# Optimization experiments

Hardware: AMD Instinct MI355X
Metric: run time of the kernel (lower is better)

## Reference

```python
import jax, jax.numpy as jnp
import numpy as np

N, M, E, HID, H = 50000, 4000, 320000, 128, 2
EPS = 1e-5  # torch BatchNorm1d eps


def _lrelu(x):
    return jnp.where(x >= 0, x, 0.2 * x)


def _bn(x, g, b):
    # BatchNorm1d in training mode: biased batch statistics over dim 0
    m = x.mean(0)
    v = ((x - m) ** 2).mean(0)
    return g * (x - m) * jax.lax.rsqrt(v + EPS) + b


def _seg_softmax(a, idx, n):
    # softmax of a[E,heads] normalized per node index idx (PyG softmax)
    mx = jax.ops.segment_max(a, idx, num_segments=n)
    e = jnp.exp(a - mx[idx])
    s = jax.ops.segment_sum(e, idx, num_segments=n)
    return e / s[idx]


def _hgconv(x, he_n, he_e, he_w, W, att, bias, heads):
    # PyG HypergraphConv(use_attention=True, concat=False)
    xl = (x @ W).reshape(N, heads, HID)                  # lin(x) -> [N,heads,C]
    # hyperedge_attr = incidence^T @ x  (matches to_dense_adj path in HGAT)
    ea = jax.ops.segment_sum(x[he_n], he_e, num_segments=M)  # [M,F]
    eal = (ea @ W).reshape(M, heads, HID)                # lin(hyperedge_attr)
    a = (jnp.concatenate([xl[he_n], eal[he_e]], axis=-1) * att[0]).sum(-1)  # [E,heads]
    a = _seg_softmax(_lrelu(a), he_n, N)
    # degree normalizations
    Dn = jax.ops.segment_sum(he_w[he_e], he_n, num_segments=N)
    Dinv = jnp.where(Dn > 0, 1.0 / Dn, 0.0)
    Bn = jax.ops.segment_sum(jnp.ones((E,), x.dtype), he_e, num_segments=M)
    Binv = jnp.where(Bn > 0, 1.0 / Bn, 0.0)
    # node -> hyperedge
    m1 = Binv[he_e][:, None, None] * xl[he_n] * a[..., None]
    eo = jax.ops.segment_sum(m1, he_e, num_segments=M)   # [M,heads,C]
    # hyperedge -> node
    m2 = Dinv[he_n][:, None, None] * eo[he_e] * a[..., None]
    out = jax.ops.segment_sum(m2, he_n, num_segments=N)  # [N,heads,C]
    return out.mean(1) + bias                            # concat=False -> head mean


def _forward(x, he_w, lin1_w, lin1_b, bn1_g, bn1_b, h1_w, h1_att, h1_b,
             bn2_g, bn2_b, h2_w, h2_att, h2_b, bn3_g, bn3_b,
             lin2_w, lin2_b, bn4_g, bn4_b, he_n, he_e):
    src = x
    x = _bn(_lrelu(x @ lin1_w + lin1_b), bn1_g, bn1_b)
    x2 = _hgconv(x, he_n, he_e, he_w, h1_w, h1_att, h1_b, H)
    x = _bn(x + x2, bn2_g, bn2_b)
    x2 = _hgconv(x, he_n, he_e, he_w, h2_w, h2_att, h2_b, 1)
    x = _bn(x + x2, bn3_g, bn3_b)
    x = _lrelu(x @ lin2_w + lin2_b)
    return _bn(src + x, bn4_g, bn4_b)


def setup_inputs() -> dict:
    key = jax.random.key(0)
    ks = jax.random.split(key, 10)
    s = 0.05
    he_n = jax.random.randint(ks[0], (E,), 0, N, dtype=jnp.int32)
    he_e = (jnp.arange(E, dtype=jnp.int32) % M)  # every hyperedge id used
    return {
        'x': jax.random.normal(ks[1], (N, 128), jnp.float32),
        'he_n': he_n, 'he_e': he_e,
        'he_w': jnp.ones((M,), jnp.float32),
        'lin1_w': jax.random.normal(ks[2], (128, HID), jnp.float32) * s,
        'lin1_b': jnp.zeros((HID,), jnp.float32),
        'bn1_g': jnp.ones((HID,), jnp.float32), 'bn1_b': jnp.zeros((HID,), jnp.float32),
        'h1_w': jax.random.normal(ks[3], (HID, H * HID), jnp.float32) * s,
        'h1_att': jax.random.normal(ks[4], (1, H, 2 * HID), jnp.float32) * s,
        'h1_b': jnp.zeros((HID,), jnp.float32),
        'bn2_g': jnp.ones((HID,), jnp.float32), 'bn2_b': jnp.zeros((HID,), jnp.float32),
        'h2_w': jax.random.normal(ks[5], (HID, HID), jnp.float32) * s,
        'h2_att': jax.random.normal(ks[6], (1, 1, 2 * HID), jnp.float32) * s,
        'h2_b': jnp.zeros((HID,), jnp.float32),
        'bn3_g': jnp.ones((HID,), jnp.float32), 'bn3_b': jnp.zeros((HID,), jnp.float32),
        'lin2_w': jax.random.normal(ks[7], (HID, 128), jnp.float32) * s,
        'lin2_b': jnp.zeros((128,), jnp.float32),
        'bn4_g': jnp.ones((128,), jnp.float32), 'bn4_b': jnp.zeros((128,), jnp.float32),
    }


def reference(x, he_n, he_e, he_w, lin1_w, lin1_b, bn1_g, bn1_b, h1_w, h1_att, h1_b,
              bn2_g, bn2_b, h2_w, h2_att, h2_b, bn3_g, bn3_b,
              lin2_w, lin2_b, bn4_g, bn4_b):
    return _forward(x, he_w, lin1_w, lin1_b, bn1_g, bn1_b, h1_w, h1_att, h1_b,
                    bn2_g, bn2_b, h2_w, h2_att, h2_b, bn3_g, bn3_b,
                    lin2_w, lin2_b, bn4_g, bn4_b, he_n, he_e)
```

## Files before the change

### kernel.cpp

```cpp
#include <hip/hip_runtime.h>
#include <math.h>

constexpr int Nn = 50000;
constexpr int Mm = 4000;
constexpr int Ee = 320000;
constexpr int KPB = Ee / Mm;
constexpr float BINV = 1.0f / (float)KPB;
constexpr float EPSf = 1e-5f;
constexpr int NBKT = 16;
constexpr int NBSCAN = 49;

__device__ __forceinline__ float lrelu_f(float x) { return x >= 0.f ? x : 0.2f * x; }

__device__ __forceinline__ float wave_sum(float v) {
#pragma unroll
    for (int o = 32; o >= 1; o >>= 1) v += __shfl_xor(v, o, 64);
    return v;
}

__device__ __forceinline__ void finalize_to_lds(const float* __restrict__ st,
                                                const float* __restrict__ g,
                                                const float* __restrict__ b,
                                                float* ABsh, int t) {
    if (t < 128) {
        double ds = 0, dq = 0;
#pragma unroll
        for (int i = 0; i < NBKT; i++) {
            ds += (double)st[i * 256 + t];
            dq += (double)st[i * 256 + 128 + t];
        }
        double mean = ds / (double)Nn;
        double var = dq / (double)Nn - mean * mean;
        float rstd = (float)(1.0 / sqrt(var + (double)EPSf));
        float A = g[t] * rstd;
        ABsh[t] = A;
        ABsh[128 + t] = b[t] - (float)mean * A;
    }
    __syncthreads();
}

__device__ void scan_body(const int* __restrict__ counts, int* __restrict__ offs,
                          int b, int t) {
    __shared__ int sdi[256];
    int pre = 0;
    for (int i = t; i < b * 1024; i += 256) pre += counts[i];
    sdi[t] = pre;
    __syncthreads();
    for (int st = 128; st >= 1; st >>= 1) {
        if (t < st) sdi[t] += sdi[t + st];
        __syncthreads();
    }
    int run0 = sdi[0];
    __syncthreads();
    int c4[4];
    int s = 0;
#pragma unroll
    for (int i = 0; i < 4; i++) {
        int n = b * 1024 + t * 4 + i;
        c4[i] = (n < Nn) ? counts[n] : 0;
        s += c4[i];
    }
    sdi[t] = s;
    __syncthreads();
    for (int off = 1; off < 256; off <<= 1) {
        int v = (t >= off) ? sdi[t - off] : 0;
        __syncthreads();
        sdi[t] += v;
        __syncthreads();
    }
    int run = sdi[t] - s + run0;
#pragma unroll
    for (int i = 0; i < 4; i++) {
        int n = b * 1024 + t * 4 + i;
        if (n < Nn) offs[n] = run;
        run += c4[i];
    }
    if (b == NBSCAN - 1 && t == 255) offs[Nn] = run0 + sdi[255];
}

template <int ROWS, bool LRELU, bool PROBN, bool RESID, bool STATS, bool PACKH2, bool SCANX>
__global__ __launch_bounds__(256) void gemmT(const float* __restrict__ A, size_t aystride,
                                             const float* __restrict__ B, int ldb,
                                             const float* __restrict__ bias, float scale,
                                             const float* __restrict__ stIn,
                                             const float* __restrict__ fing,
                                             const float* __restrict__ finb,
                                             const float* __restrict__ resid,
                                             float* __restrict__ stF,
                                             float* __restrict__ C, int ldc, int R,
                                             int gemmBlocksX,
                                             const int* __restrict__ counts,
                                             int* __restrict__ offs) {
    constexpr int RPT = ROWS / 16;
    const int t = threadIdx.x;
    if (SCANX && (int)blockIdx.x >= gemmBlocksX) {
        if (blockIdx.y == 0) scan_body(counts, offs, blockIdx.x - gemmBlocksX, t);
        return;
    }
    __shared__ float As[16][ROWS + 4];
    __shared__ float Bs[16][128];
    __shared__ float Sred[STATS ? 16 : 1][STATS ? 128 : 1];
    __shared__ float ABsh[PROBN ? 256 : 1];
    const int ty = t >> 4, tx = t & 15;
    const int row0 = blockIdx.x * ROWS;
    const int bcol = blockIdx.y * 128;
    A += (size_t)blockIdx.y * aystride;

    if (PROBN) finalize_to_lds(stIn, fing, finb, ABsh, t);

    float4 acc[RPT][2];
#pragma unroll
    for (int i = 0; i < RPT; i++)
#pragma unroll
        for (int q = 0; q < 2; q++) acc[i][q] = make_float4(0.f, 0.f, 0.f, 0.f);

    for (int k0 = 0; k0 < 128; k0 += 16) {
        if (ROWS == 64) {
            int r = t >> 2, kc = (t & 3) * 4;
            int rr = row0 + r;
            rr = rr < R ? rr : R - 1;
            float4 av = *(const float4*)(A + (size_t)rr * 128 + k0 + kc);
            if (PROBN) {
                float4 sA = *(const float4*)&ABsh[k0 + kc];
                float4 sB = *(const float4*)&ABsh[128 + k0 + kc];
                av.x = av.x * sA.x + sB.x; av.y = av.y * sA.y + sB.y;
                av.z = av.z * sA.z + sB.z; av.w = av.w * sA.w + sB.w;
            }
            As[kc + 0][r] = av.x; As[kc + 1][r] = av.y;
            As[kc + 2][r] = av.z; As[kc + 3][r] = av.w;
        } else {
            int r = t >> 3, kc = (t & 7) * 2;
            int rr = row0 + r;
            rr = rr < R ? rr : R - 1;
            float2 av = *(const float2*)(A + (size_t)rr * 128 + k0 + kc);
            if (PROBN) {
                av.x = av.x * ABsh[k0 + kc] + ABsh[128 + k0 + kc];
                av.y = av.y * ABsh[k0 + kc + 1] + ABsh[128 + k0 + kc + 1];
            }
            As[kc + 0][r] = av.x;
            As[kc + 1][r] = av.y;
        }
        {
            int kk = t >> 5, c4 = (t & 31) * 4;
            float4 bv0 = *(const float4*)(B + (size_t)(k0 + kk) * ldb + bcol + c4);
            float4 bv1 = *(const float4*)(B + (size_t)(k0 + kk + 8) * ldb + bcol + c4);
            *(float4*)&Bs[kk][c4] = bv0;
            *(float4*)&Bs[kk + 8][c4] = bv1;
        }
        __syncthreads();
#pragma unroll
        for (int kk = 0; kk < 16; kk++) {
            float ar[RPT];
            if (RPT == 4) {
                float4 a4 = *(const float4*)&As[kk][ty * 4];
                ar[0] = a4.x; ar[1] = a4.y; ar[2] = a4.z; ar[3] = a4.w;
            } else {
                float2 a2 = *(const float2*)&As[kk][ty * 2];
                ar[0] = a2.x; ar[RPT - 1] = a2.y;
            }
            float4 b0 = *(const float4*)&Bs[kk][4 * tx];
            float4 b1 = *(const float4*)&Bs[kk][64 + 4 * tx];
#pragma unroll
            for (int i = 0; i < RPT; i++) {
                acc[i][0].x = fmaf(ar[i], b0.x, acc[i][0].x);
                acc[i][0].y = fmaf(ar[i], b0.y, acc[i][0].y);
                acc[i][0].z = fmaf(ar[i], b0.z, acc[i][0].z);
                acc[i][0].w = fmaf(ar[i], b0.w, acc[i][0].w);
                acc[i][1].x = fmaf(ar[i], b1.x, acc[i][1].x);
                acc[i][1].y = fmaf(ar[i], b1.y, acc[i][1].y);
                acc[i][1].z = fmaf(ar[i], b1.z, acc[i][1].z);
                acc[i][1].w = fmaf(ar[i], b1.w, acc[i][1].w);
            }
        }
        __syncthreads();
    }

    float4 bv0 = make_float4(0.f, 0.f, 0.f, 0.f), bv1 = bv0;
    if (bias) {
        bv0 = *(const float4*)(bias + bcol + 4 * tx);
        bv1 = *(const float4*)(bias + bcol + 64 + 4 * tx);
    }
    float4 cs0 = make_float4(0.f, 0.f, 0.f, 0.f), cs1 = cs0, cq0 = cs0, cq1 = cs0;
#pragma unroll
    for (int i = 0; i < RPT; i++) {
        int row = row0 + ty * RPT + i;
        if (row >= R) continue;
        float4 v0, v1;
        v0.x = acc[i][0].x * scale + bv0.x; v0.y = acc[i][0].y * scale + bv0.y;
        v0.z = acc[i][0].z * scale + bv0.z; v0.w = acc[i][0].w * scale + bv0.w;
        v1.x = acc[i][1].x * scale + bv1.x; v1.y = acc[i][1].y * scale + bv1.y;
        v1.z = acc[i][1].z * scale + bv1.z; v1.w = acc[i][1].w * scale + bv1.w;
        if (LRELU) {
            v0.x = lrelu_f(v0.x); v0.y = lrelu_f(v0.y); v0.z = lrelu_f(v0.z); v0.w = lrelu_f(v0.w);
            v1.x = lrelu_f(v1.x); v1.y = lrelu_f(v1.y); v1.z = lrelu_f(v1.z); v1.w = lrelu_f(v1.w);
        }
        if (RESID) {
            float4 r0 = *(const float4*)(resid + (size_t)row * 128 + bcol + 4 * tx);
            float4 r1 = *(const float4*)(resid + (size_t)row * 128 + bcol + 64 + 4 * tx);
            v0.x += r0.x; v0.y += r0.y; v0.z += r0.z; v0.w += r0.w;
            v1.x += r1.x; v1.y += r1.y; v1.z += r1.z; v1.w += r1.w;
        }
        if (PACKH2) {
            int h = blockIdx.y;
            float* c0 = C + (size_t)row * ldc + 8 * tx + 2 * h;
            *(float2*)(c0) = make_float2(v0.x, v0.y);
            *(float2*)(c0 + 4) = make_float2(v0.z, v0.w);
            float* c1 = C + (size_t)row * ldc + 128 + 8 * tx + 2 * h;
            *(float2*)(c1) = make_float2(v1.x, v1.y);
            *(float2*)(c1 + 4) = make_float2(v1.z, v1.w);
        } else {
            *(float4*)(C + (size_t)row * ldc + bcol + 4 * tx) = v0;
            *(float4*)(C + (size_t)row * ldc + bcol + 64 + 4 * tx) = v1;
        }
        if (STATS) {
            cs0.x += v0.x; cs0.y += v0.y; cs0.z += v0.z; cs0.w += v0.w;
            cs1.x += v1.x; cs1.y += v1.y; cs1.z += v1.z; cs1.w += v1.w;
            cq0.x += v0.x * v0.x; cq0.y += v0.y * v0.y; cq0.z += v0.z * v0.z; cq0.w += v0.w * v0.w;
            cq1.x += v1.x * v1.x; cq1.y += v1.y * v1.y; cq1.z += v1.z * v1.z; cq1.w += v1.w * v1.w;
        }
    }
    if (STATS) {
        int bkt = blockIdx.x & (NBKT - 1);
#pragma unroll
        for (int pass = 0; pass < 2; pass++) {
            *(float4*)&Sred[ty][4 * tx] = pass ? cq0 : cs0;
            *(float4*)&Sred[ty][64 + 4 * tx] = pass ? cq1 : cs1;
            __syncthreads();
            if (t < 128) {
                float tot = 0.f;
#pragma unroll
                for (int r = 0; r < 16; r++) tot += Sred[r][t];
                atomicAdd(&stF[bkt * 256 + pass * 128 + t], tot);
            }
            __syncthreads();
        }
    }
}

__global__ void count_edges_watt(const int* __restrict__ he_n, int* __restrict__ counts,
                                 const float* __restrict__ h1_w, const float* __restrict__ h1_att,
                                 const float* __restrict__ h2_w, const float* __restrict__ h2_att,
                                 float* __restrict__ wnA, float* __restrict__ weA) {
    int t = threadIdx.x;
    if (blockIdx.x == 1250) {
        for (int j = 0; j < 3; j++) {
            int id = t + 256 * j;
            if (id >= 768) break;
            int which = id / 384;
            int rem = id % 384;
            int h3 = rem >> 7, k = rem & 127;
            float s = 0.f;
            if (h3 < 2) {
                const float* wrow = h1_w + (size_t)k * 256 + h3 * 128;
                const float* arow = h1_att + h3 * 256 + which * 128;
                for (int c = 0; c < 128; c++) s += wrow[c] * arow[c];
            } else {
                const float* wrow = h2_w + (size_t)k * 128;
                const float* arow = h2_att + which * 128;
                for (int c = 0; c < 128; c++) s += wrow[c] * arow[c];
            }
            (which ? weA : wnA)[h3 * 128 + k] = s;
        }
        return;
    }
    int e = blockIdx.x * 256 + t;
    if (e < Ee) atomicAdd(&counts[he_n[e]], 1);
}

template <int H, bool FILL>
__global__ __launch_bounds__(256) void bn_dots(const float* __restrict__ X,
                                               const float* __restrict__ stIn,
                                               const float* __restrict__ fing,
                                               const float* __restrict__ finb,
                                               float* __restrict__ ABout,
                                               const float* __restrict__ wn,
                                               const float* __restrict__ we,
                                               float* __restrict__ an,
                                               float* __restrict__ pe,
                                               const int* __restrict__ he_n,
                                               const int* __restrict__ offs,
                                               int* __restrict__ cursor,
                                               int* __restrict__ eid, int mainBlocks) {
    int t = threadIdx.x;
    if (FILL && (int)blockIdx.x >= mainBlocks) {
        int e = (blockIdx.x - mainBlocks) * 256 + t;
        if (e < Ee) {
            int n = he_n[e];
            int p = atomicAdd(&cursor[n], 1);
            eid[offs[n] + p] = e;
        }
        return;
    }
    __shared__ float ABsh[256];
    finalize_to_lds(stIn, fing, finb, ABsh, t);
    if (blockIdx.x == 0) ABout[t] = ABsh[t];
    int w = t >> 6, lane = t & 63;
    float a0 = ABsh[lane], a1 = ABsh[lane + 64];
    float b0 = ABsh[128 + lane], b1 = ABsh[192 + lane];
    float wn0[H], wn1[H], we0[H], we1[H];
#pragma unroll
    for (int h = 0; h < H; h++) {
        wn0[h] = wn[h * 128 + lane]; wn1[h] = wn[h * 128 + 64 + lane];
        we0[h] = we[h * 128 + lane]; we1[h] = we[h * 128 + 64 + lane];
    }
#pragma unroll
    for (int nn = 0; nn < 4; nn++) {
        int row = blockIdx.x * 16 + w * 4 + nn;
        const float* xr = X + (size_t)row * 128;
        float v0 = xr[lane] * a0 + b0;
        float v1 = xr[lane + 64] * a1 + b1;
        float pv[H], qv[H];
#pragma unroll
        for (int h = 0; h < H; h++) {
            pv[h] = wave_sum(v0 * wn0[h] + v1 * wn1[h]);
            qv[h] = wave_sum(v0 * we0[h] + v1 * we1[h]);
        }
        if (lane == 0) {
            if (H == 2) {
                *(float2*)&an[row * 2] = make_float2(pv[0], pv[1]);
                *(float2*)&pe[row * 2] = make_float2(qv[0], qv[1]);
            } else {
                an[row] = pv[0];
                pe[row] = qv[0];
            }
        }
    }
}

__global__ __launch_bounds__(256) void bn_out(const float* __restrict__ X,
                                              const float* __restrict__ stIn,
                                              const float* __restrict__ fing,
                                              const float* __restrict__ finb,
                                              float* __restrict__ Y) {
    __shared__ float ABsh[256];
    int t = threadIdx.x;
    finalize_to_lds(stIn, fing, finb, ABsh, t);
    int w = t >> 6, lane = t & 63;
    float a0 = ABsh[lane], a1 = ABsh[lane + 64];
    float b0 = ABsh[128 + lane], b1 = ABsh[192 + lane];
#pragma unroll
    for (int nn = 0; nn < 4; nn++) {
        int row = blockIdx.x * 16 + w * 4 + nn;
        const float* xr = X + (size_t)row * 128;
        float* yr = Y + (size_t)row * 128;
        yr[lane] = xr[lane] * a0 + b0;
        yr[lane + 64] = xr[lane + 64] * a1 + b1;
    }
}

template <int H>
__global__ __launch_bounds__(256) void ea_from_pe(const int* __restrict__ he_n,
                                                  const float* __restrict__ pe,
                                                  float* __restrict__ ae) {
    int w = threadIdx.x >> 6, lane = threadIdx.x & 63;
    int m = blockIdx.x * 4 + w;
    if (m >= Mm) return;
    float s[H];
#pragma unroll
    for (int h = 0; h < H; h++) s[h] = 0.f;
    for (int k = lane; k < KPB; k += 64) {
        int idx = he_n[m + k * Mm];
        if (H == 2) {
            float2 p2 = *(const float2*)(pe + (size_t)idx * 2);
            s[0] += p2.x;
            s[H - 1] += p2.y;
        } else {
            s[0] += pe[idx];
        }
    }
#pragma unroll
    for (int h = 0; h < H; h++) s[h] = wave_sum(s[h]);
    if (lane == 0)
#pragma unroll
        for (int h = 0; h < H; h++) ae[m * H + h] = s[h];
}

template <int H>
__global__ __launch_bounds__(256) void seg_softmax(const int* __restrict__ offs,
                                                   const int* __restrict__ eid,
                                                   const float* __restrict__ an,
                                                   const float* __restrict__ ae,
                                                   const float* __restrict__ he_w,
                                                   float* __restrict__ aw,
                                                   float* __restrict__ sdl) {
    int t = threadIdx.x;
    int wv = t >> 6, lane = t & 63;
    int q = lane >> 3, li = lane & 7;
    int n = blockIdx.x * 32 + wv * 8 + q;
    bool valid = n < Nn;
    int base = valid ? offs[n] : 0;
    int deg = valid ? offs[n + 1] - base : 0;
    float anv[H];
#pragma unroll
    for (int h = 0; h < H; h++) anv[h] = valid ? an[n * H + h] : 0.f;

    bool h0 = li < deg, h1 = li + 8 < deg;
    int e0 = 0, e1 = 0, m0 = 0, m1 = 0;
    float l0[H], l1[H];
    float mx[H];
#pragma unroll
    for (int h = 0; h < H; h++) { mx[h] = -INFINITY; l0[h] = 0.f; l1[h] = 0.f; }
    if (h0) {
        e0 = eid[base + li];
        m0 = e0 % Mm;
#pragma unroll
        for (int h = 0; h < H; h++) {
            l0[h] = lrelu_f(anv[h] + ae[m0 * H + h]);
            mx[h] = fmaxf(mx[h], l0[h]);
        }
    }
    if (h1) {
        e1 = eid[base + li + 8];
        m1 = e1 % Mm;
#pragma unroll
        for (int h = 0; h < H; h++) {
            l1[h] = lrelu_f(anv[h] + ae[m1 * H + h]);
            mx[h] = fmaxf(mx[h], l1[h]);
        }
    }
    for (int c = li + 16; c < deg; c += 8) {
        int e = eid[base + c];
        int m = e % Mm;
#pragma unroll
        for (int h = 0; h < H; h++) mx[h] = fmaxf(mx[h], lrelu_f(anv[h] + ae[m * H + h]));
    }
#pragma unroll
    for (int h = 0; h < H; h++) {
#pragma unroll
        for (int o = 1; o <= 4; o <<= 1) mx[h] = fmaxf(mx[h], __shfl_xor(mx[h], o, 64));
    }
    float sm[H], p0[H], p1[H];
#pragma unroll
    for (int h = 0; h < H; h++) { sm[h] = 0.f; p0[h] = 0.f; p1[h] = 0.f; }
    float dn = 0.f;
    if (h0) {
        dn += he_w[m0];
#pragma unroll
        for (int h = 0; h < H; h++) { p0[h] = expf(l0[h] - mx[h]); sm[h] += p0[h]; }
    }
    if (h1) {
        dn += he_w[m1];
#pragma unroll
        for (int h = 0; h < H; h++) { p1[h] = expf(l1[h] - mx[h]); sm[h] += p1[h]; }
    }
    for (int c = li + 16; c < deg; c += 8) {
        int e = eid[base + c];
        int m = e % Mm;
        dn += he_w[m];
#pragma unroll
        for (int h = 0; h < H; h++) sm[h] += expf(lrelu_f(anv[h] + ae[m * H + h]) - mx[h]);
    }
#pragma unroll
    for (int o = 1; o <= 4; o <<= 1) dn += __shfl_xor(dn, o, 64);
#pragma unroll
    for (int h = 0; h < H; h++) {
#pragma unroll
        for (int o = 1; o <= 4; o <<= 1) sm[h] += __shfl_xor(sm[h], o, 64);
    }
    float Dv = dn > 0.f ? 1.0f / dn : 0.0f;
    float premul = Dv * (H == 2 ? 0.5f : 1.0f);
    if (h0) {
        float p[H];
#pragma unroll
        for (int h = 0; h < H; h++) p[h] = p0[h] / sm[h];
        if (H == 2) {
            *(float2*)(aw + (size_t)e0 * 2) = make_float2(p[0], p[1]);
            *(float4*)(sdl + (size_t)(base + li) * 4) =
                make_float4(__int_as_float(m0), p[0] * premul, p[H - 1] * premul, 0.f);
        } else {
            aw[e0] = p[0];
            *(float2*)(sdl + (size_t)(base + li) * 2) = make_float2(__int_as_float(m0), p[0] * premul);
        }
    }
    if (h1) {
        float p[H];
#pragma unroll
        for (int h = 0; h < H; h++) p[h] = p1[h] / sm[h];
        if (H == 2) {
            *(float2*)(aw + (size_t)e1 * 2) = make_float2(p[0], p[1]);
            *(float4*)(sdl + (size_t)(base + li + 8) * 4) =
                make_float4(__int_as_float(m1), p[0] * premul, p[H - 1] * premul, 0.f);
        } else {
            aw[e1] = p[0];
            *(float2*)(sdl + (size_t)(base + li + 8) * 2) =
                make_float2(__int_as_float(m1), p[0] * premul);
        }
    }
    for (int c = li + 16; c < deg; c += 8) {
        int e = eid[base + c];
        int m = e % Mm;
        float p[H];
#pragma unroll
        for (int h = 0; h < H; h++) p[h] = expf(lrelu_f(anv[h] + ae[m * H + h]) - mx[h]) / sm[h];
        if (H == 2) {
            *(float2*)(aw + (size_t)e * 2) = make_float2(p[0], p[1]);
            *(float4*)(sdl + (size_t)(base + c) * 4) =
                make_float4(__int_as_float(m), p[0] * premul, p[H - 1] * premul, 0.f);
        } else {
            aw[e] = p[0];
            *(float2*)(sdl + (size_t)(base + c) * 2) = make_float2(__int_as_float(m), p[0] * premul);
        }
    }
}

template <int H>
__global__ __launch_bounds__(256) void s_build(const float* __restrict__ X,
                                               const float* __restrict__ AB,
                                               const int* __restrict__ he_n,
                                               const float* __restrict__ aw,
                                               float* __restrict__ S) {
    __shared__ int idx[KPB];
    __shared__ float av[KPB][H];
    __shared__ float red[8][H][128];
    int m = blockIdx.x, t = threadIdx.x;
    int g = t >> 5, l = t & 31;
    if (t < KPB) idx[t] = he_n[m + t * Mm];
    for (int q2 = t; q2 < KPB * H; q2 += 256) {
        int k = q2 / H, h = q2 - k * H;
        av[k][h] = aw[(size_t)(m + k * Mm) * H + h];
    }
    __syncthreads();
    float4 A4 = ((const float4*)AB)[l];
    float4 B4 = ((const float4*)(AB + 128))[l];
    float4 acc[H];
#pragma unroll
    for (int h = 0; h < H; h++) acc[h] = make_float4(0.f, 0.f, 0.f, 0.f);
#pragma unroll
    for (int kk = 0; kk < KPB / 8; kk++) {
        int k = g + kk * 8;
        float4 v = ((const float4*)(X + (size_t)idx[k] * 128))[l];
        v.x = v.x * A4.x + B4.x;
        v.y = v.y * A4.y + B4.y;
        v.z = v.z * A4.z + B4.z;
        v.w = v.w * A4.w + B4.w;
#pragma unroll
        for (int h = 0; h < H; h++) {
            float a = av[k][h];
            acc[h].x = fmaf(a, v.x, acc[h].x);
            acc[h].y = fmaf(a, v.y, acc[h].y);
            acc[h].z = fmaf(a, v.z, acc[h].z);
            acc[h].w = fmaf(a, v.w, acc[h].w);
        }
    }
#pragma unroll
    for (int h = 0; h < H; h++) *(float4*)&red[g][h][l * 4] = acc[h];
    __syncthreads();
    if (t < 32 * H) {
        int h = t >> 5, l2 = t & 31;
        float4 s = make_float4(0.f, 0.f, 0.f, 0.f);
#pragma unroll
        for (int gg = 0; gg < 8; gg++) {
            float4 r = *(const float4*)&red[gg][h][l2 * 4];
            s.x += r.x; s.y += r.y; s.z += r.z; s.w += r.w;
        }
        ((float4*)(S + ((size_t)h * Mm + m) * 128))[l2] = s;
    }
}

template <int H>
__global__ __launch_bounds__(256) void node_agg(const int* __restrict__ offs,
                                                const float* __restrict__ sdl,
                                                const float* __restrict__ eo,
                                                const float* __restrict__ bias,
                                                const float* __restrict__ AB,
                                                float* __restrict__ stF,
                                                float* __restrict__ T) {
    __shared__ float smem[4][256];
    __shared__ float redS[4][128], redQ[4][128];
    int t = threadIdx.x;
    int w = t >> 6, lane = t & 63;
    int n0 = blockIdx.x * 16 + w * 4;
    int o = offs[n0 + (lane < 4 ? lane : 4)];
    int b0 = __shfl(o, 0, 64);
    int b1 = __shfl(o, 1, 64);
    int b2 = __shfl(o, 2, 64);
    int b3 = __shfl(o, 3, 64);
    int b4 = __shfl(o, 4, 64);
    int cnt = b4 - b0;
    int cnt64 = cnt < 64 ? cnt : 64;

    if (lane < cnt64) {
        int slot = b0 + lane;
        if (H == 2) {
            *(float4*)&smem[w][4 * lane] = *(const float4*)(sdl + (size_t)slot * 4);
        } else {
            *(float2*)&smem[w][2 * lane] = *(const float2*)(sdl + (size_t)slot * 2);
        }
    }
    __syncthreads();

    int s1 = min(b1 - b0, cnt64), s2 = min(b2 - b0, cnt64), s3 = min(b3 - b0, cnt64);
    float2 acc0 = make_float2(0.f, 0.f), acc1 = acc0, acc2 = acc0, acc3 = acc0;

#define NA_BODY(ACC, CBEG, CEND)                                                \
    {                                                                           \
        int c = (CBEG);                                                         \
        for (; c + 1 < (CEND); c += 2) {                                        \
            if (H == 2) {                                                       \
                float4 sa = *(const float4*)&smem[w][4 * c];                    \
                float4 sb = *(const float4*)&smem[w][4 * (c + 1)];              \
                float4 ea = *(const float4*)(eo + (size_t)__float_as_int(sa.x) * 256 + 4 * lane); \
                float4 eb = *(const float4*)(eo + (size_t)__float_as_int(sb.x) * 256 + 4 * lane); \
                ACC.x += sa.y * ea.x + sa.z * ea.z + sb.y * eb.x + sb.z * eb.z; \
                ACC.y += sa.y * ea.y + sa.z * ea.w + sb.y * eb.y + sb.z * eb.w; \
            } else {                                                            \
                float2 sa = *(const float2*)&smem[w][2 * c];                    \
                float2 sb = *(const float2*)&smem[w][2 * (c + 1)];              \
                float2 ea = *(const float2*)(eo + (size_t)__float_as_int(sa.x) * 128 + 2 * lane); \
                float2 eb = *(const float2*)(eo + (size_t)__float_as_int(sb.x) * 128 + 2 * lane); \
                ACC.x += sa.y * ea.x + sb.y * eb.x;                             \
                ACC.y += sa.y * ea.y + sb.y * eb.y;                             \
            }                                                                   \
        }                                                                       \
        if (c < (CEND)) {                                                       \
            if (H == 2) {                                                       \
                float4 sa = *(const float4*)&smem[w][4 * c];                    \
                float4 ea = *(const float4*)(eo + (size_t)__float_as_int(sa.x) * 256 + 4 * lane); \
                ACC.x += sa.y * ea.x + sa.z * ea.z;                             \
                ACC.y += sa.y * ea.y + sa.z * ea.w;                             \
            } else {                                                            \
                float2 sa = *(const float2*)&smem[w][2 * c];                    \
                float2 ea = *(const float2*)(eo + (size_t)__float_as_int(sa.x) * 128 + 2 * lane); \
                ACC.x += sa.y * ea.x;                                           \
                ACC.y += sa.y * ea.y;                                           \
            }                                                                   \
        }                                                                       \
    }
    NA_BODY(acc0, 0, s1)
    NA_BODY(acc1, s1, s2)
    NA_BODY(acc2, s2, s3)
    NA_BODY(acc3, s3, cnt64)
#undef NA_BODY

    for (int ss = 64; ss < cnt; ss++) {
        int slot = b0 + ss;
        int j = (slot >= b1) + (slot >= b2) + (slot >= b3);
        float cx, cy;
        if (H == 2) {
            float4 v = *(const float4*)(sdl + (size_t)slot * 4);
            float4 ev = *(const float4*)(eo + (size_t)__float_as_int(v.x) * 256 + 4 * lane);
            cx = v.y * ev.x + v.z * ev.z;
            cy = v.y * ev.y + v.z * ev.w;
        } else {
            float2 v = *(const float2*)(sdl + (size_t)slot * 2);
            float2 ev = *(const float2*)(eo + (size_t)__float_as_int(v.x) * 128 + 2 * lane);
            cx = v.y * ev.x;
            cy = v.y * ev.y;
        }
        if (j == 0) { acc0.x += cx; acc0.y += cy; }
        else if (j == 1) { acc1.x += cx; acc1.y += cy; }
        else if (j == 2) { acc2.x += cx; acc2.y += cy; }
        else { acc3.x += cx; acc3.y += cy; }
    }

    int col = 2 * lane;
    float2 A2 = *(const float2*)(AB + col);
    float2 B2 = *(const float2*)(AB + 128 + col);
    float2 bi = *(const float2*)(bias + col);
    float cs0 = 0.f, cs1 = 0.f, cq0 = 0.f, cq1 = 0.f;
    float2 accs[4] = {acc0, acc1, acc2, acc3};
#pragma unroll
    for (int j = 0; j < 4; j++) {
        int n = n0 + j;
        float2 xr = *(const float2*)(T + (size_t)n * 128 + col);
        float r0 = xr.x * A2.x + B2.x + bi.x + accs[j].x;
        float r1 = xr.y * A2.y + B2.y + bi.y + accs[j].y;
        *(float2*)(T + (size_t)n * 128 + col) = make_float2(r0, r1);
        cs0 += r0; cs1 += r1;
        cq0 += r0 * r0; cq1 += r1 * r1;
    }
    redS[w][col] = cs0; redS[w][col + 1] = cs1;
    redQ[w][col] = cq0; redQ[w][col + 1] = cq1;
    __syncthreads();
    if (t < 128) {
        float s = 0.f, qq = 0.f;
#pragma unroll
        for (int ww = 0; ww < 4; ww++) { s += redS[ww][t]; qq += redQ[ww][t]; }
        int bkt = blockIdx.x & (NBKT - 1);
        atomicAdd(&stF[bkt * 256 + t], s);
        atomicAdd(&stF[bkt * 256 + 128 + t], qq);
    }
}

extern "C" void kernel_launch(void* const* d_in, const int* in_sizes, int n_in,
                              void* d_out, int out_size, void* d_ws, size_t ws_size,
                              hipStream_t stream) {
    const float* x = (const float*)d_in[0];
    const int* he_n = (const int*)d_in[1];
    const float* he_w = (const float*)d_in[3];
    const float* lin1_w = (const float*)d_in[4];
    const float* lin1_b = (const float*)d_in[5];
    const float* bn1_g = (const float*)d_in[6];
    const float* bn1_b = (const float*)d_in[7];
    const float* h1_w = (const float*)d_in[8];
    const float* h1_att = (const float*)d_in[9];
    const float* h1_b = (const float*)d_in[10];
    const float* bn2_g = (const float*)d_in[11];
    const float* bn2_b = (const float*)d_in[12];
    const float* h2_w = (const float*)d_in[13];
    const float* h2_att = (const float*)d_in[14];
    const float* h2_b = (const float*)d_in[15];
    const float* bn3_g = (const float*)d_in[16];
    const float* bn3_b = (const float*)d_in[17];
    const float* lin2_w = (const float*)d_in[18];
    const float* lin2_b = (const float*)d_in[19];
    const float* bn4_g = (const float*)d_in[20];
    const float* bn4_b = (const float*)d_in[21];
    float* out = (float*)d_out;

    char* ws = (char*)d_ws;
    size_t off = 0;
    auto alloc = [&](size_t bytes) -> char* {
        char* p = ws + off;
        off = (off + bytes + 255) & ~(size_t)255;
        return p;
    };
    int* counts = (int*)alloc((size_t)Nn * 4);
    int* cursor = (int*)alloc((size_t)Nn * 4);
    float* stats = (float*)alloc((size_t)4 * NBKT * 256 * 4);
    size_t zbytes = off;
    int* offs = (int*)alloc((size_t)(Nn + 1) * 4);
    int* eid = (int*)alloc((size_t)Ee * 4);
    float* an = (float*)alloc((size_t)Nn * 2 * 4);
    float* pe = (float*)alloc((size_t)Nn * 2 * 4);
    float* ae = (float*)alloc((size_t)Mm * 2 * 4);
    float* aw = (float*)alloc((size_t)Ee * 2 * 4);
    float* sdl = (float*)alloc((size_t)Ee * 4 * 4);
    float* S = (float*)alloc((size_t)2 * Mm * 128 * 4);
    float* eo = (float*)alloc((size_t)2 * Mm * 128 * 4);
    float* wnA = (float*)alloc(384 * 4);
    float* weA = (float*)alloc(384 * 4);
    float* AB = (float*)alloc(2 * 256 * 4);
    float* buf = (float*)alloc((size_t)Nn * 128 * 4);

    float* st0 = stats;
    float* st1 = stats + NBKT * 256;
    float* st2 = stats + 2 * NBKT * 256;
    float* st3 = stats + 3 * NBKT * 256;
    float *AB1 = AB, *AB2 = AB + 256;

    hipMemsetAsync(d_ws, 0, zbytes, stream);

    constexpr int GB32 = (Nn + 31) / 32;
    count_edges_watt<<<1251, 256, 0, stream>>>(he_n, counts, h1_w, h1_att, h2_w, h2_att,
                                               wnA, weA);

    gemmT<32, true, false, false, true, false, true><<<dim3(GB32 + NBSCAN, 1), 256, 0, stream>>>(
        x, 0, lin1_w, 128, lin1_b, 1.f, nullptr, nullptr, nullptr, nullptr, st0, buf, 128, Nn,
        GB32, counts, offs);
    bn_dots<2, true><<<3125 + 1250, 256, 0, stream>>>(buf, st0, bn1_g, bn1_b, AB1, wnA, weA,
                                                      an, pe, he_n, offs, cursor, eid, 3125);

    ea_from_pe<2><<<Mm / 4, 256, 0, stream>>>(he_n, pe, ae);
    seg_softmax<2><<<(Nn + 31) / 32, 256, 0, stream>>>(offs, eid, an, ae, he_w, aw, sdl);
    s_build<2><<<Mm, 256, 0, stream>>>(buf, AB1, he_n, aw, S);
    gemmT<32, false, false, false, false, true, false><<<dim3(125, 2), 256, 0, stream>>>(
        S, (size_t)Mm * 128, h1_w, 256, nullptr, BINV, nullptr, nullptr, nullptr, nullptr,
        nullptr, eo, 256, Mm, 125, nullptr, nullptr);
    node_agg<2><<<3125, 256, 0, stream>>>(offs, sdl, eo, h1_b, AB1, st1, buf);

    bn_dots<1, false><<<3125, 256, 0, stream>>>(buf, st1, bn2_g, bn2_b, AB2, wnA + 256,
                                                weA + 256, an, pe, nullptr, nullptr, nullptr,
                                                nullptr, 3125);

    ea_from_pe<1><<<Mm / 4, 256, 0, stream>>>(he_n, pe, ae);
    seg_softmax<1><<<(Nn + 31) / 32, 256, 0, stream>>>(offs, eid, an, ae, he_w, aw, sdl);
    s_build<1><<<Mm, 256, 0, stream>>>(buf, AB2, he_n, aw, S);
    gemmT<32, false, false, false, false, false, false><<<dim3(125, 1), 256, 0, stream>>>(
        S, 0, h2_w, 128, nullptr, BINV, nullptr, nullptr, nullptr, nullptr, nullptr,
        eo, 128, Mm, 125, nullptr, nullptr);
    node_agg<1><<<3125, 256, 0, stream>>>(offs, sdl, eo, h2_b, AB2, st2, buf);

    gemmT<32, true, true, true, true, false, false><<<dim3(GB32, 1), 256, 0, stream>>>(
        buf, 0, lin2_w, 128, lin2_b, 1.f, st2, bn3_g, bn3_b, x, st3, buf, 128, Nn,
        GB32, nullptr, nullptr);
    bn_out<<<3125, 256, 0, stream>>>(buf, st3, bn4_g, bn4_b, out);
}
```

Before: 399.5 us.

## Store per-node softmax stats and recompute edge attention on the fly

```diff
diff --git a/kernel.cpp b/kernel.cpp
--- a/kernel.cpp
+++ b/kernel.cpp
@@ -240,7 +240,8 @@
 __global__ void count_edges_watt(const int* __restrict__ he_n, int* __restrict__ counts,
                                  const float* __restrict__ h1_w, const float* __restrict__ h1_att,
                                  const float* __restrict__ h2_w, const float* __restrict__ h2_att,
-                                 float* __restrict__ wnA, float* __restrict__ weA) {
+                                 float* __restrict__ wnA, float* __restrict__ weA,
+                                 int* __restrict__ he_nT) {
     int t = threadIdx.x;
     if (blockIdx.x == 1250) {
         for (int j = 0; j < 3; j++) {
@@ -263,8 +264,14 @@
         }
         return;
     }
-    int e = blockIdx.x * 256 + t;
-    if (e < Ee) atomicAdd(&counts[he_n[e]], 1);
+    int g = blockIdx.x * 256 + t;
+    if (g < Ee) {
+        int m = g / KPB;
+        int k = g - m * KPB;
+        int n = he_n[m + (size_t)k * Mm];
+        he_nT[g] = n;
+        atomicAdd(&counts[n], 1);
+    }
 }
 
 template <int H, bool FILL>
@@ -349,7 +356,7 @@
 }
 
 template <int H>
-__global__ __launch_bounds__(256) void ea_from_pe(const int* __restrict__ he_n,
+__global__ __launch_bounds__(256) void ea_from_pe(const int* __restrict__ he_nT,
                                                   const float* __restrict__ pe,
                                                   float* __restrict__ ae) {
     int w = threadIdx.x >> 6, lane = threadIdx.x & 63;
@@ -359,7 +366,7 @@
 #pragma unroll
     for (int h = 0; h < H; h++) s[h] = 0.f;
     for (int k = lane; k < KPB; k += 64) {
-        int idx = he_n[m + k * Mm];
+        int idx = he_nT[m * KPB + k];
         if (H == 2) {
             float2 p2 = *(const float2*)(pe + (size_t)idx * 2);
             s[0] += p2.x;
@@ -381,8 +388,7 @@
                                                    const float* __restrict__ an,
                                                    const float* __restrict__ ae,
                                                    const float* __restrict__ he_w,
-                                                   float* __restrict__ aw,
-                                                   float* __restrict__ sdl) {
+                                                   float* __restrict__ nsp) {
     int t = threadIdx.x;
     int wv = t >> 6, lane = t & 63;
     int q = lane >> 3, li = lane & 7;
@@ -395,14 +401,13 @@
     for (int h = 0; h < H; h++) anv[h] = valid ? an[n * H + h] : 0.f;
 
     bool h0 = li < deg, h1 = li + 8 < deg;
-    int e0 = 0, e1 = 0, m0 = 0, m1 = 0;
+    int m0 = 0, m1 = 0;
     float l0[H], l1[H];
     float mx[H];
 #pragma unroll
     for (int h = 0; h < H; h++) { mx[h] = -INFINITY; l0[h] = 0.f; l1[h] = 0.f; }
     if (h0) {
-        e0 = eid[base + li];
-        m0 = e0 % Mm;
+        m0 = eid[base + li] % Mm;
 #pragma unroll
         for (int h = 0; h < H; h++) {
             l0[h] = lrelu_f(anv[h] + ae[m0 * H + h]);
@@ -410,8 +415,7 @@
         }
     }
     if (h1) {
-        e1 = eid[base + li + 8];
-        m1 = e1 % Mm;
+        m1 = eid[base + li + 8] % Mm;
 #pragma unroll
         for (int h = 0; h < H; h++) {
             l1[h] = lrelu_f(anv[h] + ae[m1 * H + h]);
@@ -419,8 +423,7 @@
         }
     }
     for (int c = li + 16; c < deg; c += 8) {
-        int e = eid[base + c];
-        int m = e % Mm;
+        int m = eid[base + c] % Mm;
 #pragma unroll
         for (int h = 0; h < H; h++) mx[h] = fmaxf(mx[h], lrelu_f(anv[h] + ae[m * H + h]));
     }
@@ -429,23 +432,22 @@
 #pragma unroll
         for (int o = 1; o <= 4; o <<= 1) mx[h] = fmaxf(mx[h], __shfl_xor(mx[h], o, 64));
     }
-    float sm[H], p0[H], p1[H];
-#pragma unroll
-    for (int h = 0; h < H; h++) { sm[h] = 0.f; p0[h] = 0.f; p1[h] = 0.f; }
+    float sm[H];
+#pragma unroll
+    for (int h = 0; h < H; h++) sm[h] = 0.f;
     float dn = 0.f;
     if (h0) {
         dn += he_w[m0];
 #pragma unroll
-        for (int h = 0; h < H; h++) { p0[h] = expf(l0[h] - mx[h]); sm[h] += p0[h]; }
+        for (int h = 0; h < H; h++) sm[h] += expf(l0[h] - mx[h]);
     }
     if (h1) {
         dn += he_w[m1];
 #pragma unroll
-        for (int h = 0; h < H; h++) { p1[h] = expf(l1[h] - mx[h]); sm[h] += p1[h]; }
+        for (int h = 0; h < H; h++) sm[h] += expf(l1[h] - mx[h]);
     }
     for (int c = li + 16; c < deg; c += 8) {
-        int e = eid[base + c];
-        int m = e % Mm;
+        int m = eid[base + c] % Mm;
         dn += he_w[m];
 #pragma unroll
         for (int h = 0; h < H; h++) sm[h] += expf(lrelu_f(anv[h] + ae[m * H + h]) - mx[h]);
@@ -457,48 +459,14 @@
 #pragma unroll
         for (int o = 1; o <= 4; o <<= 1) sm[h] += __shfl_xor(sm[h], o, 64);
     }
-    float Dv = dn > 0.f ? 1.0f / dn : 0.0f;
-    float premul = Dv * (H == 2 ? 0.5f : 1.0f);
-    if (h0) {
-        float p[H];
-#pragma unroll
-        for (int h = 0; h < H; h++) p[h] = p0[h] / sm[h];
+    if (valid && li == 0) {
+        float Dv = dn > 0.f ? 1.0f / dn : 0.0f;
         if (H == 2) {
-            *(float2*)(aw + (size_t)e0 * 2) = make_float2(p[0], p[1]);
-            *(float4*)(sdl + (size_t)(base + li) * 4) =
-                make_float4(__int_as_float(m0), p[0] * premul, p[H - 1] * premul, 0.f);
+            *(float4*)(nsp + (size_t)n * 8) = make_float4(anv[0], anv[H - 1], mx[0], mx[H - 1]);
+            *(float4*)(nsp + (size_t)n * 8 + 4) =
+                make_float4(1.f / sm[0], 1.f / sm[H - 1], 0.5f * Dv, 0.f);
         } else {
-            aw[e0] = p[0];
-            *(float2*)(sdl + (size_t)(base + li) * 2) = make_float2(__int_as_float(m0), p[0] * premul);
-        }
-    }
-    if (h1) {
-        float p[H];
-#pragma unroll
-        for (int h = 0; h < H; h++) p[h] = p1[h] / sm[h];
-        if (H == 2) {
-            *(float2*)(aw + (size_t)e1 * 2) = make_float2(p[0], p[1]);
-            *(float4*)(sdl + (size_t)(base + li + 8) * 4) =
-                make_float4(__int_as_float(m1), p[0] * premul, p[H - 1] * premul, 0.f);
-        } else {
-            aw[e1] = p[0];
-            *(float2*)(sdl + (size_t)(base + li + 8) * 2) =
-                make_float2(__int_as_float(m1), p[0] * premul);
-        }
-    }
-    for (int c = li + 16; c < deg; c += 8) {
-        int e = eid[base + c];
-        int m = e % Mm;
-        float p[H];
-#pragma unroll
-        for (int h = 0; h < H; h++) p[h] = expf(lrelu_f(anv[h] + ae[m * H + h]) - mx[h]) / sm[h];
-        if (H == 2) {
-            *(float2*)(aw + (size_t)e * 2) = make_float2(p[0], p[1]);
-            *(float4*)(sdl + (size_t)(base + c) * 4) =
-                make_float4(__int_as_float(m), p[0] * premul, p[H - 1] * premul, 0.f);
-        } else {
-            aw[e] = p[0];
-            *(float2*)(sdl + (size_t)(base + c) * 2) = make_float2(__int_as_float(m), p[0] * premul);
+            *(float4*)(nsp + (size_t)n * 4) = make_float4(anv[0], mx[0], 1.f / sm[0], Dv);
         }
     }
 }
@@ -506,18 +474,29 @@
 template <int H>
 __global__ __launch_bounds__(256) void s_build(const float* __restrict__ X,
                                                const float* __restrict__ AB,
-                                               const int* __restrict__ he_n,
-                                               const float* __restrict__ aw,
+                                               const int* __restrict__ he_nT,
+                                               const float* __restrict__ nsp,
+                                               const float* __restrict__ ae,
                                                float* __restrict__ S) {
     __shared__ int idx[KPB];
     __shared__ float av[KPB][H];
     __shared__ float red[8][H][128];
     int m = blockIdx.x, t = threadIdx.x;
     int g = t >> 5, l = t & 31;
-    if (t < KPB) idx[t] = he_n[m + t * Mm];
-    for (int q2 = t; q2 < KPB * H; q2 += 256) {
-        int k = q2 / H, h = q2 - k * H;
-        av[k][h] = aw[(size_t)(m + k * Mm) * H + h];
+    if (t < KPB) {
+        int nd = he_nT[m * KPB + t];
+        idx[t] = nd;
+        if (H == 2) {
+            float4 pa = *(const float4*)(nsp + (size_t)nd * 8);
+            float4 pb = *(const float4*)(nsp + (size_t)nd * 8 + 4);
+            float2 a2 = *(const float2*)(ae + (size_t)m * 2);
+            av[t][0] = expf(lrelu_f(pa.x + a2.x) - pa.z) * pb.x;
+            av[t][H - 1] = expf(lrelu_f(pa.y + a2.y) - pa.w) * pb.y;
+        } else {
+            float4 pa = *(const float4*)(nsp + (size_t)nd * 4);
+            float aem = ae[m];
+            av[t][0] = expf(lrelu_f(pa.x + aem) - pa.y) * pa.z;
+        }
     }
     __syncthreads();
     float4 A4 = ((const float4*)AB)[l];
@@ -559,7 +538,9 @@
 
 template <int H>
 __global__ __launch_bounds__(256) void node_agg(const int* __restrict__ offs,
-                                                const float* __restrict__ sdl,
+                                                const int* __restrict__ eid,
+                                                const float* __restrict__ nsp,
+                                                const float* __restrict__ ae,
                                                 const float* __restrict__ eo,
                                                 const float* __restrict__ bias,
                                                 const float* __restrict__ AB,
@@ -581,10 +562,20 @@
 
     if (lane < cnt64) {
         int slot = b0 + lane;
+        int j = (slot >= b1) + (slot >= b2) + (slot >= b3);
+        int e = eid[slot];
+        int m = e % Mm;
         if (H == 2) {
-            *(float4*)&smem[w][4 * lane] = *(const float4*)(sdl + (size_t)slot * 4);
+            float4 pa = *(const float4*)(nsp + (size_t)(n0 + j) * 8);
+            float4 pb = *(const float4*)(nsp + (size_t)(n0 + j) * 8 + 4);
+            float2 a2 = *(const float2*)(ae + (size_t)m * 2);
+            float c0 = expf(lrelu_f(pa.x + a2.x) - pa.z) * pb.x * pb.z;
+            float c1 = expf(lrelu_f(pa.y + a2.y) - pa.w) * pb.y * pb.z;
+            *(float4*)&smem[w][4 * lane] = make_float4(__int_as_float(m), c0, c1, 0.f);
         } else {
-            *(float2*)&smem[w][2 * lane] = *(const float2*)(sdl + (size_t)slot * 2);
+            float4 pa = *(const float4*)(nsp + (size_t)(n0 + j) * 4);
+            float c = expf(lrelu_f(pa.x + ae[m]) - pa.y) * pa.z * pa.w;
+            *(float2*)&smem[w][2 * lane] = make_float2(__int_as_float(m), c);
         }
     }
     __syncthreads();
@@ -635,17 +626,24 @@
     for (int ss = 64; ss < cnt; ss++) {
         int slot = b0 + ss;
         int j = (slot >= b1) + (slot >= b2) + (slot >= b3);
+        int e = eid[slot];
+        int m = e % Mm;
         float cx, cy;
         if (H == 2) {
-            float4 v = *(const float4*)(sdl + (size_t)slot * 4);
-            float4 ev = *(const float4*)(eo + (size_t)__float_as_int(v.x) * 256 + 4 * lane);
-            cx = v.y * ev.x + v.z * ev.z;
-            cy = v.y * ev.y + v.z * ev.w;
+            float4 pa = *(const float4*)(nsp + (size_t)(n0 + j) * 8);
+            float4 pb = *(const float4*)(nsp + (size_t)(n0 + j) * 8 + 4);
+            float2 a2 = *(const float2*)(ae + (size_t)m * 2);
+            float c0 = expf(lrelu_f(pa.x + a2.x) - pa.z) * pb.x * pb.z;
+            float c1 = expf(lrelu_f(pa.y + a2.y) - pa.w) * pb.y * pb.z;
+            float4 ev = *(const float4*)(eo + (size_t)m * 256 + 4 * lane);
+            cx = c0 * ev.x + c1 * ev.z;
+            cy = c0 * ev.y + c1 * ev.w;
         } else {
-            float2 v = *(const float2*)(sdl + (size_t)slot * 2);
-            float2 ev = *(const float2*)(eo + (size_t)__float_as_int(v.x) * 128 + 2 * lane);
-            cx = v.y * ev.x;
-            cy = v.y * ev.y;
+            float4 pa = *(const float4*)(nsp + (size_t)(n0 + j) * 4);
+            float c = expf(lrelu_f(pa.x + ae[m]) - pa.y) * pa.z * pa.w;
+            float2 ev = *(const float2*)(eo + (size_t)m * 128 + 2 * lane);
+            cx = c * ev.x;
+            cy = c * ev.y;
         }
         if (j == 0) { acc0.x += cx; acc0.y += cy; }
         else if (j == 1) { acc1.x += cx; acc1.y += cy; }
@@ -721,11 +719,11 @@
     size_t zbytes = off;
     int* offs = (int*)alloc((size_t)(Nn + 1) * 4);
     int* eid = (int*)alloc((size_t)Ee * 4);
+    int* he_nT = (int*)alloc((size_t)Ee * 4);
     float* an = (float*)alloc((size_t)Nn * 2 * 4);
     float* pe = (float*)alloc((size_t)Nn * 2 * 4);
     float* ae = (float*)alloc((size_t)Mm * 2 * 4);
-    float* aw = (float*)alloc((size_t)Ee * 2 * 4);
-    float* sdl = (float*)alloc((size_t)Ee * 4 * 4);
+    float* nsp = (float*)alloc((size_t)Nn * 8 * 4);
     float* S = (float*)alloc((size_t)2 * Mm * 128 * 4);
     float* eo = (float*)alloc((size_t)2 * Mm * 128 * 4);
     float* wnA = (float*)alloc(384 * 4);
@@ -743,7 +741,7 @@
 
     constexpr int GB32 = (Nn + 31) / 32;
     count_edges_watt<<<1251, 256, 0, stream>>>(he_n, counts, h1_w, h1_att, h2_w, h2_att,
-                                               wnA, weA);
+                                               wnA, weA, he_nT);
 
     gemmT<32, true, false, false, true, false, true><<<dim3(GB32 + NBSCAN, 1), 256, 0, stream>>>(
         x, 0, lin1_w, 128, lin1_b, 1.f, nullptr, nullptr, nullptr, nullptr, st0, buf, 128, Nn,
@@ -751,25 +749,25 @@
     bn_dots<2, true><<<3125 + 1250, 256, 0, stream>>>(buf, st0, bn1_g, bn1_b, AB1, wnA, weA,
                                                       an, pe, he_n, offs, cursor, eid, 3125);
 
-    ea_from_pe<2><<<Mm / 4, 256, 0, stream>>>(he_n, pe, ae);
-    seg_softmax<2><<<(Nn + 31) / 32, 256, 0, stream>>>(offs, eid, an, ae, he_w, aw, sdl);
-    s_build<2><<<Mm, 256, 0, stream>>>(buf, AB1, he_n, aw, S);
+    ea_from_pe<2><<<Mm / 4, 256, 0, stream>>>(he_nT, pe, ae);
+    seg_softmax<2><<<(Nn + 31) / 32, 256, 0, stream>>>(offs, eid, an, ae, he_w, nsp);
+    s_build<2><<<Mm, 256, 0, stream>>>(buf, AB1, he_nT, nsp, ae, S);
     gemmT<32, false, false, false, false, true, false><<<dim3(125, 2), 256, 0, stream>>>(
         S, (size_t)Mm * 128, h1_w, 256, nullptr, BINV, nullptr, nullptr, nullptr, nullptr,
         nullptr, eo, 256, Mm, 125, nullptr, nullptr);
-    node_agg<2><<<3125, 256, 0, stream>>>(offs, sdl, eo, h1_b, AB1, st1, buf);
+    node_agg<2><<<3125, 256, 0, stream>>>(offs, eid, nsp, ae, eo, h1_b, AB1, st1, buf);
 
     bn_dots<1, false><<<3125, 256, 0, stream>>>(buf, st1, bn2_g, bn2_b, AB2, wnA + 256,
                                                 weA + 256, an, pe, nullptr, nullptr, nullptr,
                                                 nullptr, 3125);
 
-    ea_from_pe<1><<<Mm / 4, 256, 0, stream>>>(he_n, pe, ae);
-    seg_softmax<1><<<(Nn + 31) / 32, 256, 0, stream>>>(offs, eid, an, ae, he_w, aw, sdl);
-    s_build<1><<<Mm, 256, 0, stream>>>(buf, AB2, he_n, aw, S);
+    ea_from_pe<1><<<Mm / 4, 256, 0, stream>>>(he_nT, pe, ae);
+    seg_softmax<1><<<(Nn + 31) / 32, 256, 0, stream>>>(offs, eid, an, ae, he_w, nsp);
+    s_build<1><<<Mm, 256, 0, stream>>>(buf, AB2, he_nT, nsp, ae, S);
     gemmT<32, false, false, false, false, false, false><<<dim3(125, 1), 256, 0, stream>>>(
         S, 0, h2_w, 128, nullptr, BINV, nullptr, nullptr, nullptr, nullptr, nullptr,
         eo, 128, Mm, 125, nullptr, nullptr);
-    node_agg<1><<<3125, 256, 0, stream>>>(offs, sdl, eo, h2_b, AB2, st2, buf);
+    node_agg<1><<<3125, 256, 0, stream>>>(offs, eid, nsp, ae, eo, h2_b, AB2, st2, buf);
 
     gemmT<32, true, true, true, true, false, false><<<dim3(GB32, 1), 256, 0, stream>>>(
         buf, 0, lin2_w, 128, lin2_b, 1.f, st2, bn3_g, bn3_b, x, st3, buf, 128, Nn,
```

Measured after the change: 394.0 us. Within noise of the previous version (-1.4%).
